# Kernel optimization log

Measured on AMD Instinct MI355X. Metric: run time of the kernel, lower is better.

The kernel has to match this reference:

```python
import jax, jax.numpy as jnp
import numpy as np
import math

B, I, C = 64, 512, 32
PRED, PL, ST, NH = 96, 16, 8, 8
WKS = (24, 168, 336)
PN = (I + ST - PL) // ST + 1  # 64 patches (padding_patch='end')

def _gelu(x):
    return jax.nn.gelu(x, approximate=False)  # torch nn.GELU default (erf)

def _ln(x, g, b, eps=1e-5):
    m = x.mean(-1, keepdims=True)
    v = ((x - m) ** 2).mean(-1, keepdims=True)
    return (x - m) / jnp.sqrt(v + eps) * g + b

def setup_inputs() -> dict:
    keys = jax.random.split(jax.random.key(0), 64)
    ki = iter(keys)
    def nrm(sh, sc=0.02):
        return (jax.random.normal(next(ki), sh) * sc).astype(jnp.float32)
    inp = {}
    inp['s'] = jax.random.normal(next(ki), (B, I, C), jnp.float32)
    inp['t'] = jax.random.normal(next(ki), (B, I, C), jnp.float32)
    inp['cycle_index'] = jax.random.randint(next(ki), (B,), 0, 336)
    # router: Linear(C, C//2) -> GELU -> Linear(C//2, num_scales)
    inp['rw1'] = nrm((C // 2, C)); inp['rb1'] = jnp.zeros(C // 2)
    inp['rw2'] = nrm((3, C // 2)); inp['rb2'] = jnp.zeros(3)
    # per-scale amplitude / phase tables (Wk, C)
    inp['A0'] = nrm((WKS[0], C), 1.0); inp['A1'] = nrm((WKS[1], C), 1.0); inp['A2'] = nrm((WKS[2], C), 1.0)
    inp['P0'] = (jax.random.uniform(next(ki), (WKS[0], C)) * 2 * math.pi).astype(jnp.float32)
    inp['P1'] = (jax.random.uniform(next(ki), (WKS[1], C)) * 2 * math.pi).astype(jnp.float32)
    inp['P2'] = (jax.random.uniform(next(ki), (WKS[2], C)) * 2 * math.pi).astype(jnp.float32)
    # PB_RPA (phase-biased relative patch attention), n_embd=PL, n_head=NH
    inp['Wqkv'] = nrm((3 * PL, PL)); inp['bqkv'] = jnp.zeros(3 * PL)
    inp['Wo'] = nrm((PL, PL)); inp['bo'] = jnp.zeros(PL)
    inp['alpha'] = jnp.ones(())
    # bn2 over channel dim = patch_num
    inp['bn_g'] = jnp.ones(PN); inp['bn_b'] = jnp.zeros(PN)
    inp['W3'] = nrm((2 * PRED, PN * PL)); inp['b3'] = jnp.zeros(2 * PRED)
    inp['W4'] = nrm((PRED, 2 * PRED)); inp['b4'] = jnp.zeros(PRED)
    inp['W5'] = nrm((4 * PRED, I)); inp['b5'] = jnp.zeros(4 * PRED)
    inp['W6'] = nrm((PRED, 2 * PRED)); inp['b6'] = jnp.zeros(PRED)
    inp['W7'] = nrm((PRED, PRED // 2)); inp['b7'] = jnp.zeros(PRED)
    inp['W8'] = nrm((PRED, 2 * PRED)); inp['b8'] = jnp.zeros(PRED)
    inp['ln1_g'] = jnp.ones(2 * PRED); inp['ln1_b'] = jnp.zeros(2 * PRED)
    inp['ln2_g'] = jnp.ones(PRED // 2); inp['ln2_b'] = jnp.zeros(PRED // 2)
    # TrendEnhancer: Conv1d(C, C, 3, pad=1) gated residual
    inp['te_w'] = nrm((C, C, 3)); inp['te_b'] = jnp.zeros(C)
    return inp

def _forward(s, t, cycle_index, rw1, rb1, rw2, rb2, A0, A1, A2, P0, P1, P2,
             Wqkv, bqkv, Wo, bo, alpha, bn_g, bn_b, W3, b3, W4, b4, W5, b5,
             W6, b6, W7, b7, W8, b8, ln1_g, ln1_b, ln2_g, ln2_b, te_w, te_b):
    s = s.transpose(0, 2, 1)  # (B,C,I)
    t = t.transpose(0, 2, 1)
    # router -> per-scale softmax weights (B, num_scales)
    h = _gelu(s.mean(-1) @ rw1.T + rb1)
    p = jax.nn.softmax(h @ rw2.T + rb2, axis=-1)
    ar = jnp.arange(I)
    cs, ps = [], []
    for Atab, Ptab, Wk in ((A0, P0, WKS[0]), (A1, P1, WKS[1]), (A2, P2, WKS[2])):
        idx = (cycle_index[:, None] + ar) % Wk            # (B,I) data-dependent gather
        A = jax.nn.softplus(Atab[idx]).transpose(0, 2, 1)  # (B,C,I)
        phi = Ptab[idx].transpose(0, 2, 1)
        Qr = A * jnp.cos(phi)                              # Qi=A*sin(phi) is unused in hermitian_attn
        S = jnp.einsum('bcl,bck->blk', Qr, s) / math.sqrt(C)
        Aw = jax.nn.softmax(S, axis=-1)
        cs.append(jnp.einsum('blk,bck->bcl', Aw, s))
        ps.append(phi)
    c_stack = jnp.stack(cs, 1)    # (B,3,C,I)
    phi_stack = jnp.stack(ps, 1)
    beta = p[:, :, None, None]
    s = s + (beta * c_stack).sum(1)
    fused_phi = (beta * phi_stack).sum(1)  # (B,C,I)
    N = B * C
    s = s.reshape(N, I)
    t = t.reshape(N, I)
    phi = jnp.repeat(fused_phi.mean(1), C, axis=0)  # (N,I)
    # padding_patch='end' -> replicate-pad last `stride` steps
    s = jnp.concatenate([s, jnp.repeat(s[:, -1:], ST, 1)], 1)
    phi = jnp.concatenate([phi, jnp.repeat(phi[:, -1:], ST, 1)], 1)
    widx = jnp.arange(PN)[:, None] * ST + jnp.arange(PL)
    sp = s[:, widx]                # (N, PN, PL) unfold
    phis = phi[:, widx].mean(-1)   # (N, PN)
    # PB_RPA: MHA over patches with phase-difference bias
    qkv = sp @ Wqkv.T + bqkv
    q, k, v = jnp.split(qkv, 3, axis=-1)
    hd = PL // NH
    def heads(x):
        return x.reshape(N, PN, NH, hd).transpose(0, 2, 1, 3)
    q, k, v = heads(q), heads(k), heads(v)
    bias = alpha * jnp.cos(phis[:, None, :, None] - phis[:, None, None, :])  # (N,1,PN,PN)
    sc = jnp.einsum('nhtd,nhsd->nhts', q, k) / math.sqrt(hd) + bias
    Aw = jax.nn.softmax(sc, axis=-1)
    o = jnp.einsum('nhts,nhsd->nhtd', Aw, v).transpose(0, 2, 1, 3).reshape(N, PN, PL)
    o = o @ Wo.T + bo
    sx = _gelu(sp + o)
    # bn2: BatchNorm1d over channel=patch_num (training-mode batch stats)
    mu = sx.mean((0, 2), keepdims=True)
    var = ((sx - mu) ** 2).mean((0, 2), keepdims=True)
    sx = (sx - mu) / jnp.sqrt(var + 1e-5) * bn_g[None, :, None] + bn_b[None, :, None]
    sx = sx.reshape(N, PN * PL)
    sx = _gelu(sx @ W3.T + b3) @ W4.T + b4  # (N, PRED)
    # trend branch
    u = t @ W5.T + b5                       # (N, 4*PRED)
    u = u.reshape(N, 2 * PRED, 2).mean(-1)  # AvgPool1d(2)
    u = _ln(u, ln1_g, ln1_b)
    u = u @ W6.T + b6
    u = u.reshape(N, PRED // 2, 2).mean(-1)
    u = _ln(u, ln2_g, ln2_b)
    u = u @ W7.T + b7                       # (N, PRED)
    u = u.reshape(B, C, PRED)
    f = jnp.fft.rfft(u, axis=-1)
    mask = (jnp.arange(f.shape[-1]) < 5).astype(f.dtype)
    u = u + jnp.fft.irfft(f * mask, n=PRED, axis=-1)
    y = jax.lax.conv_general_dilated(u, te_w, (1,), [(1, 1)],
                                     dimension_numbers=('NCH', 'OIH', 'NCH')) + te_b[None, :, None]
    u = (u + _gelu(y)).reshape(N, PRED)     # TrendEnhancer gated-conv residual
    x = jnp.concatenate([sx, u], 1) @ W8.T + b8
    return x.reshape(B, C, PRED).transpose(0, 2, 1)  # (B, pred_len, C)

def reference(s, t, cycle_index, rw1, rb1, rw2, rb2, A0, A1, A2, P0, P1, P2,
              Wqkv, bqkv, Wo, bo, alpha, bn_g, bn_b, W3, b3, W4, b4, W5, b5,
              W6, b6, W7, b7, W8, b8, ln1_g, ln1_b, ln2_g, ln2_b, te_w, te_b):
    return _forward(s, t, cycle_index, rw1, rb1, rw2, rb2, A0, A1, A2, P0, P1, P2,
                    Wqkv, bqkv, Wo, bo, alpha, bn_g, bn_b, W3, b3, W4, b4, W5, b5,
                    W6, b6, W7, b7, W8, b8, ln1_g, ln1_b, ln2_g, ln2_b, te_w, te_b)
```

## Files before the change

kernel.cpp:

```cpp
#include <hip/hip_runtime.h>
#include <math.h>

#define B_    64
#define I_    512
#define C_    32
#define PRED_ 96
#define PL_   16
#define ST_   8
#define NH_   8
#define PN_   64
#define N_    2048

typedef short bf16x8 __attribute__((ext_vector_type(8)));
typedef float f32x4 __attribute__((ext_vector_type(4)));
typedef bf16x8 __attribute__((may_alias)) bf16x8_a;
typedef uint2 __attribute__((may_alias)) uint2_a;
typedef uint4 __attribute__((may_alias)) uint4_a;

__device__ __forceinline__ float geluf(float x) {
    return 0.5f * x * (1.0f + erff(x * 0.70710678118654752f));
}
__device__ __forceinline__ float softplusf(float x) {
    return fmaxf(x, 0.0f) + log1pf(__expf(-fabsf(x)));
}
__device__ __forceinline__ unsigned short f2bf(float x) {
    union { float f; unsigned int u; } v; v.f = x;
    unsigned int r = v.u + 0x7fffu + ((v.u >> 16) & 1u);
    return (unsigned short)(r >> 16);
}

__global__ void k_headphi(const float* __restrict__ s, const float* __restrict__ rw1,
                          const float* __restrict__ rb1, const float* __restrict__ rw2,
                          const float* __restrict__ rb2,
                          const float* __restrict__ P0, const float* __restrict__ P1,
                          const float* __restrict__ P2, const int* __restrict__ cyc,
                          float* __restrict__ wp, float* __restrict__ phis) {
    int b = blockIdx.x, t = threadIdx.x;
    __shared__ float part[8][32];
    __shared__ float smean[32];
    __shared__ float h[16];
    __shared__ float wpl[3];
    __shared__ float pm[I_];
    int c = t & 31, chunk = t >> 5;
    float acc = 0.f;
    for (int l = chunk * 64; l < chunk * 64 + 64; ++l)
        acc += s[((size_t)b * I_ + l) * C_ + c];
    part[chunk][c] = acc;
    __syncthreads();
    if (t < 32) {
        float v = 0.f;
#pragma unroll
        for (int i = 0; i < 8; ++i) v += part[i][t];
        smean[t] = v * (1.0f / I_);
    }
    __syncthreads();
    if (t < 16) {
        float a = rb1[t];
#pragma unroll
        for (int c2 = 0; c2 < 32; ++c2) a += smean[c2] * rw1[t * 32 + c2];
        h[t] = geluf(a);
    }
    __syncthreads();
    if (t == 0) {
        float lg[3], mx = -1e30f;
        for (int k = 0; k < 3; ++k) {
            float a = rb2[k];
            for (int j = 0; j < 16; ++j) a += h[j] * rw2[k * 16 + j];
            lg[k] = a; mx = fmaxf(mx, a);
        }
        float d = 0.f;
        for (int k = 0; k < 3; ++k) { lg[k] = __expf(lg[k] - mx); d += lg[k]; }
        float inv = 1.f / d;
        for (int k = 0; k < 3; ++k) { wpl[k] = lg[k] * inv; wp[b * 3 + k] = lg[k] * inv; }
    }
    __syncthreads();
    float p0 = wpl[0], p1 = wpl[1], p2 = wpl[2];
    int cy = cyc[b];
    for (int l = t; l < I_; l += 256) {
        float acc2 = 0.f;
        {
            int idx = (cy + l) % 24;
            const float4* r = (const float4*)(P0 + idx * 32);
            float s4 = 0.f;
#pragma unroll
            for (int i = 0; i < 8; ++i) { float4 v = r[i]; s4 += v.x + v.y + v.z + v.w; }
            acc2 += p0 * s4;
        }
        {
            int idx = (cy + l) % 168;
            const float4* r = (const float4*)(P1 + idx * 32);
            float s4 = 0.f;
#pragma unroll
            for (int i = 0; i < 8; ++i) { float4 v = r[i]; s4 += v.x + v.y + v.z + v.w; }
            acc2 += p1 * s4;
        }
        {
            int idx = (cy + l) % 336;
            const float4* r = (const float4*)(P2 + idx * 32);
            float s4 = 0.f;
#pragma unroll
            for (int i = 0; i < 8; ++i) { float4 v = r[i]; s4 += v.x + v.y + v.z + v.w; }
            acc2 += p2 * s4;
        }
        pm[l] = acc2 * (1.0f / 32.0f);
    }
    __syncthreads();
    if (t < PN_) {
        float sum = 0.f;
#pragma unroll
        for (int j = 0; j < 16; ++j) {
            int l = t * ST_ + j; if (l > 511) l = 511;
            sum += pm[l];
        }
        phis[b * PN_ + t] = sum * (1.0f / 16.0f);
    }
}

__global__ void __launch_bounds__(512) k_attn_mfma(
        const float* __restrict__ s, const int* __restrict__ cyc,
        const float* __restrict__ A0, const float* __restrict__ A1, const float* __restrict__ A2,
        const float* __restrict__ P0, const float* __restrict__ P1, const float* __restrict__ P2,
        const float* __restrict__ wp, float* __restrict__ pcs) {
    int k3 = blockIdx.x, b = blockIdx.y;
    int t = threadIdx.x;
    int wid = t >> 6, lane = t & 63;
    int l15 = lane & 15, lg = lane >> 4;

    __shared__ unsigned short s_lds[512][40];
    __shared__ unsigned short sT[32][520];
    __shared__ unsigned short Pt[8][64][40];

    {
        int row = t;
        const float4* src = (const float4*)(s + ((size_t)b * I_ + row) * C_);
        unsigned short bv[32];
#pragma unroll
        for (int i = 0; i < 8; ++i) {
            float4 v = src[i];
            bv[4 * i + 0] = f2bf(v.x); bv[4 * i + 1] = f2bf(v.y);
            bv[4 * i + 2] = f2bf(v.z); bv[4 * i + 3] = f2bf(v.w);
        }
#pragma unroll
        for (int i = 0; i < 4; ++i) {
            uint4 pk;
            pk.x = (unsigned)bv[8 * i + 0] | ((unsigned)bv[8 * i + 1] << 16);
            pk.y = (unsigned)bv[8 * i + 2] | ((unsigned)bv[8 * i + 3] << 16);
            pk.z = (unsigned)bv[8 * i + 4] | ((unsigned)bv[8 * i + 5] << 16);
            pk.w = (unsigned)bv[8 * i + 6] | ((unsigned)bv[8 * i + 7] << 16);
            *((uint4_a*)&s_lds[row][8 * i]) = pk;
        }
#pragma unroll
        for (int cc = 0; cc < 32; ++cc) sT[cc][row] = bv[cc];
    }

    const float* Atab; const float* Ptab; int Wk;
    if (k3 == 0)      { Atab = A0; Ptab = P0; Wk = 24;  }
    else if (k3 == 1) { Atab = A1; Ptab = P1; Wk = 168; }
    else              { Atab = A2; Ptab = P2; Wk = 336; }
    float wpv = wp[b * 3 + k3];
    int cy = cyc[b];
    bf16x8 qrf[4];
#pragma unroll
    for (int qt = 0; qt < 4; ++qt) {
        int q = wid * 64 + qt * 16 + l15;
        int idx = (cy + q) % Wk;
        const float4* Ar = (const float4*)(Atab + idx * 32 + lg * 8);
        const float4* Pr = (const float4*)(Ptab + idx * 32 + lg * 8);
        float4 a0 = Ar[0], a1 = Ar[1], p0 = Pr[0], p1 = Pr[1];
        float qv[8];
        qv[0] = softplusf(a0.x) * __cosf(p0.x);
        qv[1] = softplusf(a0.y) * __cosf(p0.y);
        qv[2] = softplusf(a0.z) * __cosf(p0.z);
        qv[3] = softplusf(a0.w) * __cosf(p0.w);
        qv[4] = softplusf(a1.x) * __cosf(p1.x);
        qv[5] = softplusf(a1.y) * __cosf(p1.y);
        qv[6] = softplusf(a1.z) * __cosf(p1.z);
        qv[7] = softplusf(a1.w) * __cosf(p1.w);
        bf16x8 f;
#pragma unroll
        for (int j = 0; j < 8; ++j) f[j] = (short)f2bf(qv[j]);
        qrf[qt] = f;
    }
    __syncthreads();

    const float rs = 0.17677669529663687f;
    f32x4 acc[4][2];
#pragma unroll
    for (int qt = 0; qt < 4; ++qt)
#pragma unroll
        for (int ct = 0; ct < 2; ++ct) acc[qt][ct] = (f32x4){0.f, 0.f, 0.f, 0.f};
    float dacc[4] = {0.f, 0.f, 0.f, 0.f};

    for (int kc = 0; kc < 16; ++kc) {
        int key0 = kc * 32;
        bf16x8 a0 = *((const bf16x8_a*)&s_lds[key0 + l15][lg * 8]);
        bf16x8 a1 = *((const bf16x8_a*)&s_lds[key0 + 16 + l15][lg * 8]);
        f32x4 stv[4][2];
#pragma unroll
        for (int qt = 0; qt < 4; ++qt) {
            stv[qt][0] = __builtin_amdgcn_mfma_f32_16x16x32_bf16(a0, qrf[qt], (f32x4){0.f,0.f,0.f,0.f}, 0, 0, 0);
            stv[qt][1] = __builtin_amdgcn_mfma_f32_16x16x32_bf16(a1, qrf[qt], (f32x4){0.f,0.f,0.f,0.f}, 0, 0, 0);
        }
#pragma unroll
        for (int qt = 0; qt < 4; ++qt) {
#pragma unroll
            for (int h = 0; h < 2; ++h) {
                unsigned short pb[4];
                float ds = 0.f;
#pragma unroll
                for (int r = 0; r < 4; ++r) {
                    float e = __expf(stv[qt][h][r] * rs);
                    unsigned short ub = f2bf(e);
                    pb[r] = ub;
                    union { unsigned int u; float f; } bb; bb.u = ((unsigned int)ub) << 16;
                    ds += bb.f;
                }
                dacc[qt] += ds;
                uint2 w2;
                w2.x = (unsigned)pb[0] | ((unsigned)pb[1] << 16);
                w2.y = (unsigned)pb[2] | ((unsigned)pb[3] << 16);
                *((uint2_a*)&Pt[wid][qt * 16 + l15][h * 16 + lg * 4]) = w2;
            }
        }
        bf16x8 b0 = *((const bf16x8_a*)&sT[l15][key0 + lg * 8]);
        bf16x8 b1 = *((const bf16x8_a*)&sT[16 + l15][key0 + lg * 8]);
#pragma unroll
        for (int qt = 0; qt < 4; ++qt) {
            bf16x8 pa = *((const bf16x8_a*)&Pt[wid][qt * 16 + l15][lg * 8]);
            acc[qt][0] = __builtin_amdgcn_mfma_f32_16x16x32_bf16(pa, b0, acc[qt][0], 0, 0, 0);
            acc[qt][1] = __builtin_amdgcn_mfma_f32_16x16x32_bf16(pa, b1, acc[qt][1], 0, 0, 0);
        }
    }

#pragma unroll
    for (int qt = 0; qt < 4; ++qt) {
        float dq = dacc[qt];
        dq += __shfl_xor(dq, 16);
        dq += __shfl_xor(dq, 32);
        float invd[4];
#pragma unroll
        for (int r = 0; r < 4; ++r) {
            float dr = __shfl(dq, 4 * lg + r);
            invd[r] = wpv / dr;
        }
        int qbase = wid * 64 + qt * 16 + 4 * lg;
#pragma unroll
        for (int ct = 0; ct < 2; ++ct) {
            int c = ct * 16 + l15;
            float4 o;
            o.x = acc[qt][ct][0] * invd[0];
            o.y = acc[qt][ct][1] * invd[1];
            o.z = acc[qt][ct][2] * invd[2];
            o.w = acc[qt][ct][3] * invd[3];
            *(float4*)(pcs + (((size_t)k3 * B_ + b) * C_ + c) * I_ + qbase) = o;
        }
    }
}

__global__ void k_combine(const float* __restrict__ s, const float* __restrict__ t,
                          const float* __restrict__ pcs,
                          float* __restrict__ srow, float* __restrict__ trow) {
    int b = blockIdx.x, l0 = blockIdx.y * 32;
    int tt_ = threadIdx.x;
    __shared__ float st[32][33], tl[32][33];
#pragma unroll
    for (int r = 0; r < 4; ++r) {
        int lin = r * 256 + tt_;
        int lq = lin >> 5, c = lin & 31;
        st[lq][c] = s[((size_t)b * I_ + l0 + lq) * C_ + c];
        tl[lq][c] = t[((size_t)b * I_ + l0 + lq) * C_ + c];
    }
    __syncthreads();
    const size_t CH = (size_t)B_ * C_ * I_;
#pragma unroll
    for (int r = 0; r < 4; ++r) {
        int lin = r * 256 + tt_;
        int co = lin >> 5, lo = lin & 31;
        size_t pi = ((size_t)b * C_ + co) * I_ + l0 + lo;
        float sum = pcs[pi] + pcs[CH + pi] + pcs[2 * CH + pi];
        size_t oi = ((size_t)(b * C_ + co)) * I_ + l0 + lo;
        srow[oi] = st[lo][co] + sum;
        trow[oi] = tl[lo][co];
    }
}

__global__ void __launch_bounds__(256) k_patch(
        const float* __restrict__ srow, const float* __restrict__ phis,
        const float* __restrict__ Wqkv, const float* __restrict__ bqkv,
        const float* __restrict__ Wo, const float* __restrict__ bo,
        const float* __restrict__ alpha_p, float* __restrict__ sx) {
    int n = blockIdx.x, t = threadIdx.x;
    int p = t & 63, w = t >> 6;
    int b = n >> 5;
    __shared__ float spl[64][17];
    __shared__ float ql[64][17], kl[64][17], vl[64][17];
    __shared__ float cosl[64], sinl[64];
    __shared__ float wq[48][16];
    __shared__ float wo[16][16];
    __shared__ float o2l[64][17];
    float alpha = alpha_p[0];
    for (int i = t; i < 768; i += 256) wq[i >> 4][i & 15] = Wqkv[i];
    if (t < 256) wo[t >> 4][t & 15] = Wo[t];
    if (t < 64) {
        float sv, cv;
        __sincosf(phis[b * PN_ + t], &sv, &cv);
        cosl[t] = cv; sinl[t] = sv;
    }
    const float* srn = srow + (size_t)n * I_;
#pragma unroll
    for (int jj = 0; jj < 4; ++jj) {
        int j = w * 4 + jj;
        int l = p * ST_ + j; if (l > 511) l = 511;
        spl[p][j] = srn[l];
    }
    __syncthreads();
#pragma unroll
    for (int oo = 0; oo < 12; ++oo) {
        int o = w * 12 + oo;
        float a = bqkv[o];
#pragma unroll
        for (int i2 = 0; i2 < 16; ++i2) a += spl[p][i2] * wq[o][i2];
        if (o < 16) ql[p][o] = a;
        else if (o < 32) kl[p][o - 16] = a;
        else vl[p][o - 32] = a;
    }
    __syncthreads();
    const float rs2 = 0.70710678118654752f;
    float cp = alpha * cosl[p], sp_ = alpha * sinl[p];
#pragma unroll
    for (int hh = 0; hh < 2; ++hh) {
        int h = 2 * w + hh;
        float q0 = ql[p][2 * h] * rs2, q1 = ql[p][2 * h + 1] * rs2;
        float dh = 0.f, o0 = 0.f, o1 = 0.f;
        for (int ss = 0; ss < 64; ++ss) {
            float sc = q0 * kl[ss][2 * h] + q1 * kl[ss][2 * h + 1]
                     + cp * cosl[ss] + sp_ * sinl[ss];
            float e = __expf(sc);
            dh += e; o0 += e * vl[ss][2 * h]; o1 += e * vl[ss][2 * h + 1];
        }
        float inv = 1.f / dh;
        o2l[p][2 * h] = o0 * inv; o2l[p][2 * h + 1] = o1 * inv;
    }
    __syncthreads();
    float* sxr = sx + ((size_t)n * PN_ + p) * PL_;
#pragma unroll
    for (int ii = 0; ii < 4; ++ii) {
        int i2 = w * 4 + ii;
        float a = bo[i2];
#pragma unroll
        for (int j = 0; j < 16; ++j) a += o2l[p][j] * wo[i2][j];
        sxr[i2] = geluf(spl[p][i2] + a);
    }
}

__global__ void k_bn_stats(const float* __restrict__ sx, float* __restrict__ bnpart) {
    int pn = blockIdx.x, chunk = blockIdx.y, t = threadIdx.x;
    __shared__ float r1[256], r2[256];
    int j4 = t & 3, nb = t >> 2;
    float s1 = 0.f, s2 = 0.f;
    for (int i = 0; i < 8; ++i) {
        int n = chunk * 512 + nb + i * 64;
        float4 v = *(const float4*)(sx + ((size_t)n * PN_ + pn) * PL_ + j4 * 4);
        s1 += v.x + v.y + v.z + v.w;
        s2 += v.x * v.x + v.y * v.y + v.z * v.z + v.w * v.w;
    }
    r1[t] = s1; r2[t] = s2;
    __syncthreads();
    for (int st = 128; st > 0; st >>= 1) {
        if (t < st) { r1[t] += r1[t + st]; r2[t] += r2[t + st]; }
        __syncthreads();
    }
    if (t == 0) {
        bnpart[(pn * 4 + chunk) * 2 + 0] = r1[0];
        bnpart[(pn * 4 + chunk) * 2 + 1] = r2[0];
    }
}

__global__ void k_bn_final(const float* __restrict__ bnpart, const float* __restrict__ g,
                           const float* __restrict__ bb, float* __restrict__ bnmul,
                           float* __restrict__ bnadd) {
    int pn = threadIdx.x;
    float s1 = 0.f, s2 = 0.f;
#pragma unroll
    for (int ch = 0; ch < 4; ++ch) {
        s1 += bnpart[(pn * 4 + ch) * 2 + 0];
        s2 += bnpart[(pn * 4 + ch) * 2 + 1];
    }
    const float inv = 1.0f / (N_ * PL_);
    float mu = s1 * inv;
    float var = s2 * inv - mu * mu;
    float m = rsqrtf(var + 1e-5f) * g[pn];
    bnmul[pn] = m;
    bnadd[pn] = bb[pn] - mu * m;
}

template <int ACT, int FUSE_BN>
__global__ void __launch_bounds__(256) k_gemm_mfma(
        const float* __restrict__ A, const float* __restrict__ W,
        const float* __restrict__ bias, const float* __restrict__ bnmul,
        const float* __restrict__ bnadd, float* __restrict__ Cout,
        int M, int Nn, int K) {
    __shared__ unsigned short Ab[64][36];
    __shared__ unsigned short Wb[64][36];
    int bm = blockIdx.x * 64, bn = blockIdx.y * 64;
    int t = threadIdx.x;
    int wid = t >> 6, lane = t & 63, l15 = lane & 15, lg = lane >> 4;
    int srw = t >> 2, sk = (t & 3) * 8;
    f32x4 acc[4];
#pragma unroll
    for (int nt = 0; nt < 4; ++nt) acc[nt] = (f32x4){0.f, 0.f, 0.f, 0.f};

    for (int kt = 0; kt < K; kt += 32) {
        float4 av0 = *(const float4*)(A + (size_t)(bm + srw) * K + kt + sk);
        float4 av1 = *(const float4*)(A + (size_t)(bm + srw) * K + kt + sk + 4);
        float4 wv0 = *(const float4*)(W + (size_t)(bn + srw) * K + kt + sk);
        float4 wv1 = *(const float4*)(W + (size_t)(bn + srw) * K + kt + sk + 4);
        if (FUSE_BN) {
            int pn = (kt + sk) >> 4;
            float m = bnmul[pn], ad = bnadd[pn];
            av0.x = av0.x * m + ad; av0.y = av0.y * m + ad;
            av0.z = av0.z * m + ad; av0.w = av0.w * m + ad;
            av1.x = av1.x * m + ad; av1.y = av1.y * m + ad;
            av1.z = av1.z * m + ad; av1.w = av1.w * m + ad;
        }
        __syncthreads();
        {
            uint4 pk;
            pk.x = (unsigned)f2bf(av0.x) | ((unsigned)f2bf(av0.y) << 16);
            pk.y = (unsigned)f2bf(av0.z) | ((unsigned)f2bf(av0.w) << 16);
            pk.z = (unsigned)f2bf(av1.x) | ((unsigned)f2bf(av1.y) << 16);
            pk.w = (unsigned)f2bf(av1.z) | ((unsigned)f2bf(av1.w) << 16);
            *((uint4_a*)&Ab[srw][sk]) = pk;
            uint4 pw;
            pw.x = (unsigned)f2bf(wv0.x) | ((unsigned)f2bf(wv0.y) << 16);
            pw.y = (unsigned)f2bf(wv0.z) | ((unsigned)f2bf(wv0.w) << 16);
            pw.z = (unsigned)f2bf(wv1.x) | ((unsigned)f2bf(wv1.y) << 16);
            pw.w = (unsigned)f2bf(wv1.z) | ((unsigned)f2bf(wv1.w) << 16);
            *((uint4_a*)&Wb[srw][sk]) = pw;
        }
        __syncthreads();
        bf16x8 af = *((const bf16x8_a*)&Ab[wid * 16 + l15][lg * 8]);
#pragma unroll
        for (int nt = 0; nt < 4; ++nt) {
            bf16x8 wf = *((const bf16x8_a*)&Wb[nt * 16 + l15][lg * 8]);
            acc[nt] = __builtin_amdgcn_mfma_f32_16x16x32_bf16(af, wf, acc[nt], 0, 0, 0);
        }
    }
#pragma unroll
    for (int nt = 0; nt < 4; ++nt) {
#pragma unroll
        for (int r = 0; r < 4; ++r) {
            int m_ = bm + wid * 16 + 4 * lg + r;
            int n_ = bn + nt * 16 + l15;
            float v = acc[nt][r] + bias[n_];
            if (ACT) v = geluf(v);
            Cout[(size_t)m_ * Nn + n_] = v;
        }
    }
}

__global__ void k_rowmlp4(const float* __restrict__ g3, const float* __restrict__ W4,
                          const float* __restrict__ b4, float* __restrict__ sxf) {
    int n = blockIdx.x, t = threadIdx.x;
    __shared__ float row[192];
    for (int j = t; j < 192; j += 128) row[j] = g3[(size_t)n * 192 + j];
    __syncthreads();
    if (t < 96) {
        float a = b4[t];
        const float* wr = W4 + t * 192;
#pragma unroll 4
        for (int j = 0; j < 192; ++j) a += row[j] * wr[j];
        sxf[(size_t)n * 96 + t] = a;
    }
}

__global__ void k_u(const float* __restrict__ u1, const float* __restrict__ ln1g,
                    const float* __restrict__ ln1b, const float* __restrict__ W6,
                    const float* __restrict__ b6, const float* __restrict__ ln2g,
                    const float* __restrict__ ln2b, const float* __restrict__ W7,
                    const float* __restrict__ b7, float* __restrict__ u2out) {
    int n = blockIdx.x, t = threadIdx.x;
    __shared__ float a[192];
    __shared__ float red1[256], red2[256];
    __shared__ float c2[48];
    __shared__ float stat[2];
    __shared__ float u3l[96];
    __shared__ float cosb[5][96], sinb[5][96];
    __shared__ float coef[9];
    if (t < 96) {
#pragma unroll
        for (int k = 0; k < 5; ++k) {
            float sv, cv2;
            __sincosf(6.283185307179586f * (float)(k * t) / 96.0f, &sv, &cv2);
            cosb[k][t] = cv2; sinb[k][t] = sv;
        }
    }
    const float* ur = u1 + (size_t)n * 384;
    float av = 0.5f * (ur[2 * t] + ur[2 * t + 1]);
    red1[t] = av; red2[t] = av * av;
    if (t < 64) { red1[192 + t] = 0.f; red2[192 + t] = 0.f; }
    __syncthreads();
    for (int st = 128; st > 0; st >>= 1) {
        if (t < st) { red1[t] += red1[t + st]; red2[t] += red2[t + st]; }
        __syncthreads();
    }
    if (t == 0) {
        float mu = red1[0] * (1.0f / 192.0f);
        float var = red2[0] * (1.0f / 192.0f) - mu * mu;
        stat[0] = mu; stat[1] = rsqrtf(var + 1e-5f);
    }
    __syncthreads();
    a[t] = (av - stat[0]) * stat[1] * ln1g[t] + ln1b[t];
    __syncthreads();
    float bv = 0.f;
    if (t < 96) {
        bv = b6[t];
        const float* wr = W6 + t * 192;
#pragma unroll 4
        for (int j = 0; j < 192; ++j) bv += a[j] * wr[j];
    }
    __syncthreads();
    if (t < 96) red1[t] = bv;
    __syncthreads();
    float cv = 0.f;
    if (t < 48) cv = 0.5f * (red1[2 * t] + red1[2 * t + 1]);
    __syncthreads();
    if (t < 48) { red1[t] = cv; red2[t] = cv * cv; }
    else if (t < 64) { red1[t] = 0.f; red2[t] = 0.f; }
    __syncthreads();
    for (int st = 32; st > 0; st >>= 1) {
        if (t < st) { red1[t] += red1[t + st]; red2[t] += red2[t + st]; }
        __syncthreads();
    }
    if (t == 0) {
        float mu = red1[0] * (1.0f / 48.0f);
        float var = red2[0] * (1.0f / 48.0f) - mu * mu;
        stat[0] = mu; stat[1] = rsqrtf(var + 1e-5f);
    }
    __syncthreads();
    if (t < 48) c2[t] = (cv - stat[0]) * stat[1] * ln2g[t] + ln2b[t];
    __syncthreads();
    if (t < 96) {
        float acc = b7[t];
        const float* wr = W7 + t * 48;
#pragma unroll
        for (int j = 0; j < 48; ++j) acc += c2[j] * wr[j];
        u3l[t] = acc;
    }
    __syncthreads();
    if (t < 9) {
        int k = (t < 5) ? t : t - 4;
        const float* bas = (t < 5) ? cosb[k] : sinb[k];
        float acc = 0.f;
#pragma unroll 4
        for (int m = 0; m < 96; ++m) acc += u3l[m] * bas[m];
        coef[t] = acc;
    }
    __syncthreads();
    if (t < 96) {
        float rec = coef[0];
#pragma unroll
        for (int k = 1; k <= 4; ++k)
            rec += 2.0f * (coef[k] * cosb[k][t] + coef[4 + k] * sinb[k][t]);
        u2out[(size_t)n * 96 + t] = u3l[t] + rec * (1.0f / 96.0f);
    }
}

__global__ void k_conv(const float* __restrict__ u2, const float* __restrict__ tw,
                       const float* __restrict__ tb, float* __restrict__ u4) {
    int b = blockIdx.x, xq = blockIdx.y, t = threadIdx.x;
    int x0 = xq * 24;
    __shared__ float ub[32][26];
    __shared__ float twl[3072];
    for (int i = t; i < 832; i += 256) {
        int ic = i / 26, xx = i % 26;
        int gx = x0 + xx - 1;
        ub[ic][xx] = (gx >= 0 && gx < 96) ? u2[((size_t)b * 32 + ic) * 96 + gx] : 0.f;
    }
    for (int i = t; i < 3072; i += 256) twl[i] = tw[i];
    __syncthreads();
    for (int i = t; i < 768; i += 256) {
        int oc = i / 24, xx = i % 24;
        float acc = tb[oc];
#pragma unroll 8
        for (int ic = 0; ic < 32; ++ic) {
            const float* wv = twl + (oc * 32 + ic) * 3;
            acc += ub[ic][xx] * wv[0] + ub[ic][xx + 1] * wv[1] + ub[ic][xx + 2] * wv[2];
        }
        u4[((size_t)b * 32 + oc) * 96 + x0 + xx] = ub[oc][xx + 1] + geluf(acc);
    }
}

__global__ void k_out(const float* __restrict__ sxf, const float* __restrict__ u4,
                      const float* __restrict__ W8, const float* __restrict__ b8,
                      float* __restrict__ out) {
    int b = blockIdx.x, oq = blockIdx.y, t = threadIdx.x;
    __shared__ float ld[32][193];
    for (int i = t; i < 32 * 96; i += 256) {
        int c = i / 96, j = i % 96;
        ld[c][j]      = sxf[((size_t)(b * 32 + c)) * 96 + j];
        ld[c][96 + j] = u4[((size_t)(b * 32 + c)) * 96 + j];
    }
    __syncthreads();
    for (int i = t; i < 24 * 32; i += 256) {
        int o = oq * 24 + (i >> 5), c = i & 31;
        float acc = b8[o];
        const float* wr = W8 + o * 192;
#pragma unroll 4
        for (int j = 0; j < 192; ++j) acc += ld[c][j] * wr[j];
        out[((size_t)b * 96 + o) * 32 + c] = acc;
    }
}

extern "C" void kernel_launch(void* const* d_in, const int* in_sizes, int n_in,
                              void* d_out, int out_size, void* d_ws, size_t ws_size,
                              hipStream_t stream) {
    const float* s    = (const float*)d_in[0];
    const float* t    = (const float*)d_in[1];
    const int*   cyc  = (const int*)d_in[2];
    const float* rw1  = (const float*)d_in[3];
    const float* rb1  = (const float*)d_in[4];
    const float* rw2  = (const float*)d_in[5];
    const float* rb2  = (const float*)d_in[6];
    const float* A0   = (const float*)d_in[7];
    const float* A1   = (const float*)d_in[8];
    const float* A2   = (const float*)d_in[9];
    const float* P0   = (const float*)d_in[10];
    const float* P1   = (const float*)d_in[11];
    const float* P2   = (const float*)d_in[12];
    const float* Wqkv = (const float*)d_in[13];
    const float* bqkv = (const float*)d_in[14];
    const float* Wo   = (const float*)d_in[15];
    const float* bo   = (const float*)d_in[16];
    const float* alpha= (const float*)d_in[17];
    const float* bn_g = (const float*)d_in[18];
    const float* bn_b = (const float*)d_in[19];
    const float* W3   = (const float*)d_in[20];
    const float* b3   = (const float*)d_in[21];
    const float* W4   = (const float*)d_in[22];
    const float* b4   = (const float*)d_in[23];
    const float* W5   = (const float*)d_in[24];
    const float* b5   = (const float*)d_in[25];
    const float* W6   = (const float*)d_in[26];
    const float* b6   = (const float*)d_in[27];
    const float* W7   = (const float*)d_in[28];
    const float* b7   = (const float*)d_in[29];
    const float* W8   = (const float*)d_in[30];
    const float* b8   = (const float*)d_in[31];
    const float* ln1g = (const float*)d_in[32];
    const float* ln1b = (const float*)d_in[33];
    const float* ln2g = (const float*)d_in[34];
    const float* ln2b = (const float*)d_in[35];
    const float* tew  = (const float*)d_in[36];
    const float* teb  = (const float*)d_in[37];

    float* ws     = (float*)d_ws;
    float* wp     = ws;
    float* phis   = ws + 192;
    float* bnpart = ws + 4288;
    float* bnmul  = ws + 4800;
    float* bnadd  = ws + 4864;
    float* srow   = ws + 4928;
    float* trow   = srow + 1048576;
    float* R      = trow + 1048576;
    float* pcs = R;
    float* sx  = R;
    float* g3  = R + 2097152;
    float* sxf = R + 2490368;
    float* u1  = R + 2686976;
    float* u2f = R + 3473408;
    float* u4f = R + 3670016;
    float* out = (float*)d_out;

    k_headphi<<<64, 256, 0, stream>>>(s, rw1, rb1, rw2, rb2, P0, P1, P2, cyc, wp, phis);
    k_attn_mfma<<<dim3(3, 64), 512, 0, stream>>>(s, cyc, A0, A1, A2, P0, P1, P2, wp, pcs);
    k_combine<<<dim3(64, 16), 256, 0, stream>>>(s, t, pcs, srow, trow);
    k_patch<<<2048, 256, 0, stream>>>(srow, phis, Wqkv, bqkv, Wo, bo, alpha, sx);
    k_bn_stats<<<dim3(64, 4), 256, 0, stream>>>(sx, bnpart);
    k_bn_final<<<1, 64, 0, stream>>>(bnpart, bn_g, bn_b, bnmul, bnadd);
    k_gemm_mfma<1, 1><<<dim3(32, 3), 256, 0, stream>>>(sx, W3, b3, bnmul, bnadd, g3, 2048, 192, 1024);
    k_rowmlp4<<<2048, 128, 0, stream>>>(g3, W4, b4, sxf);
    k_gemm_mfma<0, 0><<<dim3(32, 6), 256, 0, stream>>>(trow, W5, b5, bnmul, bnadd, u1, 2048, 384, 512);
    k_u<<<2048, 192, 0, stream>>>(u1, ln1g, ln1b, W6, b6, ln2g, ln2b, W7, b7, u2f);
    k_conv<<<dim3(64, 4), 256, 0, stream>>>(u2f, tew, teb, u4f);
    k_out<<<dim3(64, 4), 256, 0, stream>>>(sxf, u4f, W8, b8, out);
}
```

Baseline: 351.6 us.

## Use MFMA for patch attention, fuse BN finalize, read t transposed in GEMM

The patch-attention kernel now computes the QKV projection and the attention scores with bf16 MFMA instructions instead of scalar FP32 loops. The phase bias is folded into the score MFMA as extra K columns. The BN finalize kernel is removed and its per-channel scale and shift are computed inside the GEMM prologue. The t transpose copy is dropped, and the W5 GEMM reads t directly with strided loads. This cuts launches and memory traffic but adds bf16 rounding in attention and uncoalesced strided loads in the second GEMM.

```diff
diff --git a/kernel.cpp b/kernel.cpp
--- a/kernel.cpp
+++ b/kernel.cpp
@@ -257,18 +257,16 @@
     }
 }
 
-__global__ void k_combine(const float* __restrict__ s, const float* __restrict__ t,
-                          const float* __restrict__ pcs,
-                          float* __restrict__ srow, float* __restrict__ trow) {
+__global__ void k_combine(const float* __restrict__ s, const float* __restrict__ pcs,
+                          float* __restrict__ srow) {
     int b = blockIdx.x, l0 = blockIdx.y * 32;
     int tt_ = threadIdx.x;
-    __shared__ float st[32][33], tl[32][33];
+    __shared__ float st[32][33];
 #pragma unroll
     for (int r = 0; r < 4; ++r) {
         int lin = r * 256 + tt_;
         int lq = lin >> 5, c = lin & 31;
         st[lq][c] = s[((size_t)b * I_ + l0 + lq) * C_ + c];
-        tl[lq][c] = t[((size_t)b * I_ + l0 + lq) * C_ + c];
     }
     __syncthreads();
     const size_t CH = (size_t)B_ * C_ * I_;
@@ -278,9 +276,7 @@
         int co = lin >> 5, lo = lin & 31;
         size_t pi = ((size_t)b * C_ + co) * I_ + l0 + lo;
         float sum = pcs[pi] + pcs[CH + pi] + pcs[2 * CH + pi];
-        size_t oi = ((size_t)(b * C_ + co)) * I_ + l0 + lo;
-        srow[oi] = st[lo][co] + sum;
-        trow[oi] = tl[lo][co];
+        srow[pi] = st[lo][co] + sum;
     }
 }
 
@@ -291,57 +287,125 @@
         const float* __restrict__ alpha_p, float* __restrict__ sx) {
     int n = blockIdx.x, t = threadIdx.x;
     int p = t & 63, w = t >> 6;
+    int lane = t & 63, l15 = lane & 15, lg = lane >> 4;
     int b = n >> 5;
     __shared__ float spl[64][17];
-    __shared__ float ql[64][17], kl[64][17], vl[64][17];
-    __shared__ float cosl[64], sinl[64];
-    __shared__ float wq[48][16];
+    __shared__ unsigned short spb[64][16];
+    __shared__ unsigned short wqb[48][16];
+    __shared__ unsigned short qkv2[36][72];
+    __shared__ float vlf[16][68];
+    __shared__ float o2l[64][18];
     __shared__ float wo[16][16];
-    __shared__ float o2l[64][17];
+    const float rs2 = 0.70710678118654752f;
+
     float alpha = alpha_p[0];
-    for (int i = t; i < 768; i += 256) wq[i >> 4][i & 15] = Wqkv[i];
-    if (t < 256) wo[t >> 4][t & 15] = Wo[t];
+    const float* srn = srow + (size_t)n * I_;
+#pragma unroll
+    for (int jj = 0; jj < 4; ++jj) {
+        int j = w * 4 + jj;
+        int l = p * ST_ + j; if (l > 511) l = 511;
+        float v = srn[l];
+        spl[p][j] = v; spb[p][j] = f2bf(v);
+    }
+    for (int i = t; i < 768; i += 256) wqb[i >> 4][i & 15] = f2bf(Wqkv[i]);
+    wo[t >> 4][t & 15] = Wo[t];
     if (t < 64) {
         float sv, cv;
         __sincosf(phis[b * PN_ + t], &sv, &cv);
-        cosl[t] = cv; sinl[t] = sv;
-    }
-    const float* srn = srow + (size_t)n * I_;
-#pragma unroll
-    for (int jj = 0; jj < 4; ++jj) {
-        int j = w * 4 + jj;
-        int l = p * ST_ + j; if (l > 511) l = 511;
-        spl[p][j] = srn[l];
-    }
-    __syncthreads();
-#pragma unroll
-    for (int oo = 0; oo < 12; ++oo) {
-        int o = w * 12 + oo;
-        float a = bqkv[o];
-#pragma unroll
-        for (int i2 = 0; i2 < 16; ++i2) a += spl[p][i2] * wq[o][i2];
-        if (o < 16) ql[p][o] = a;
-        else if (o < 32) kl[p][o - 16] = a;
-        else vl[p][o - 32] = a;
-    }
-    __syncthreads();
-    const float rs2 = 0.70710678118654752f;
-    float cp = alpha * cosl[p], sp_ = alpha * sinl[p];
+        qkv2[32][t] = f2bf(cv); qkv2[33][t] = f2bf(sv);
+        qkv2[34][t] = f2bf(alpha * cv); qkv2[35][t] = f2bf(alpha * sv);
+    }
+    __syncthreads();
+
+    {
+        bf16x8 af = {};
+        if (lg < 2) af = *((const bf16x8_a*)&spb[w * 16 + l15][lg * 8]);
+        f32x4 pacc[3];
+#pragma unroll
+        for (int nt = 0; nt < 3; ++nt) {
+            bf16x8 wf = {};
+            if (lg < 2) wf = *((const bf16x8_a*)&wqb[nt * 16 + l15][lg * 8]);
+            pacc[nt] = __builtin_amdgcn_mfma_f32_16x16x32_bf16(af, wf, (f32x4){0.f,0.f,0.f,0.f}, 0, 0, 0);
+        }
+        __syncthreads();
+#pragma unroll
+        for (int nt = 0; nt < 3; ++nt) {
+            int o = nt * 16 + l15;
+            float bias = bqkv[o];
+            float v0 = pacc[nt][0] + bias, v1 = pacc[nt][1] + bias;
+            float v2 = pacc[nt][2] + bias, v3 = pacc[nt][3] + bias;
+            int pb_ = w * 16 + 4 * lg;
+            if (o < 16) {
+                v0 *= rs2; v1 *= rs2; v2 *= rs2; v3 *= rs2;
+                uint2 w2;
+                w2.x = (unsigned)f2bf(v0) | ((unsigned)f2bf(v1) << 16);
+                w2.y = (unsigned)f2bf(v2) | ((unsigned)f2bf(v3) << 16);
+                *((uint2_a*)&qkv2[o][pb_]) = w2;
+            } else if (o < 32) {
+                uint2 w2;
+                w2.x = (unsigned)f2bf(v0) | ((unsigned)f2bf(v1) << 16);
+                w2.y = (unsigned)f2bf(v2) | ((unsigned)f2bf(v3) << 16);
+                *((uint2_a*)&qkv2[o][pb_]) = w2;
+            } else {
+                *(float4*)&vlf[o - 32][pb_] = make_float4(v0, v1, v2, v3);
+            }
+        }
+    }
+    __syncthreads();
+
 #pragma unroll
     for (int hh = 0; hh < 2; ++hh) {
         int h = 2 * w + hh;
-        float q0 = ql[p][2 * h] * rs2, q1 = ql[p][2 * h + 1] * rs2;
-        float dh = 0.f, o0 = 0.f, o1 = 0.f;
-        for (int ss = 0; ss < 64; ++ss) {
-            float sc = q0 * kl[ss][2 * h] + q1 * kl[ss][2 * h + 1]
-                     + cp * cosl[ss] + sp_ * sinl[ss];
-            float e = __expf(sc);
-            dh += e; o0 += e * vl[ss][2 * h]; o1 += e * vl[ss][2 * h + 1];
-        }
-        float inv = 1.f / dh;
-        o2l[p][2 * h] = o0 * inv; o2l[p][2 * h + 1] = o1 * inv;
-    }
-    __syncthreads();
+        bf16x8 qf[4];
+#pragma unroll
+        for (int pt = 0; pt < 4; ++pt) {
+            bf16x8 f = {};
+            if (lg == 0) {
+                int col = pt * 16 + l15;
+                f[0] = (short)qkv2[2 * h][col];
+                f[1] = (short)qkv2[2 * h + 1][col];
+                f[2] = (short)qkv2[34][col];
+                f[3] = (short)qkv2[35][col];
+            }
+            qf[pt] = f;
+        }
+        float o0a[4] = {0.f,0.f,0.f,0.f}, o1a[4] = {0.f,0.f,0.f,0.f}, da[4] = {0.f,0.f,0.f,0.f};
+#pragma unroll
+        for (int st = 0; st < 4; ++st) {
+            bf16x8 kf = {};
+            if (lg == 0) {
+                int col = st * 16 + l15;
+                kf[0] = (short)qkv2[16 + 2 * h][col];
+                kf[1] = (short)qkv2[17 + 2 * h][col];
+                kf[2] = (short)qkv2[32][col];
+                kf[3] = (short)qkv2[33][col];
+            }
+            float4 v0 = *(const float4*)&vlf[2 * h][st * 16 + 4 * lg];
+            float4 v1 = *(const float4*)&vlf[2 * h + 1][st * 16 + 4 * lg];
+#pragma unroll
+            for (int pt = 0; pt < 4; ++pt) {
+                f32x4 sv = __builtin_amdgcn_mfma_f32_16x16x32_bf16(kf, qf[pt], (f32x4){0.f,0.f,0.f,0.f}, 0, 0, 0);
+                float e0 = __expf(sv[0]), e1 = __expf(sv[1]);
+                float e2 = __expf(sv[2]), e3 = __expf(sv[3]);
+                da[pt] += e0 + e1 + e2 + e3;
+                o0a[pt] += e0 * v0.x + e1 * v0.y + e2 * v0.z + e3 * v0.w;
+                o1a[pt] += e0 * v1.x + e1 * v1.y + e2 * v1.z + e3 * v1.w;
+            }
+        }
+#pragma unroll
+        for (int pt = 0; pt < 4; ++pt) {
+            float o0 = o0a[pt], o1 = o1a[pt], dd = da[pt];
+            o0 += __shfl_xor(o0, 16); o0 += __shfl_xor(o0, 32);
+            o1 += __shfl_xor(o1, 16); o1 += __shfl_xor(o1, 32);
+            dd += __shfl_xor(dd, 16); dd += __shfl_xor(dd, 32);
+            if (lg == 0) {
+                float inv = 1.f / dd;
+                *(float2*)&o2l[pt * 16 + l15][2 * h] = make_float2(o0 * inv, o1 * inv);
+            }
+        }
+    }
+    __syncthreads();
+
     float* sxr = sx + ((size_t)n * PN_ + p) * PL_;
 #pragma unroll
     for (int ii = 0; ii < 4; ++ii) {
@@ -376,48 +440,56 @@
     }
 }
 
-__global__ void k_bn_final(const float* __restrict__ bnpart, const float* __restrict__ g,
-                           const float* __restrict__ bb, float* __restrict__ bnmul,
-                           float* __restrict__ bnadd) {
-    int pn = threadIdx.x;
-    float s1 = 0.f, s2 = 0.f;
-#pragma unroll
-    for (int ch = 0; ch < 4; ++ch) {
-        s1 += bnpart[(pn * 4 + ch) * 2 + 0];
-        s2 += bnpart[(pn * 4 + ch) * 2 + 1];
-    }
-    const float inv = 1.0f / (N_ * PL_);
-    float mu = s1 * inv;
-    float var = s2 * inv - mu * mu;
-    float m = rsqrtf(var + 1e-5f) * g[pn];
-    bnmul[pn] = m;
-    bnadd[pn] = bb[pn] - mu * m;
-}
-
-template <int ACT, int FUSE_BN>
+template <int ACT, int FUSE_BN, int TRANS>
 __global__ void __launch_bounds__(256) k_gemm_mfma(
         const float* __restrict__ A, const float* __restrict__ W,
-        const float* __restrict__ bias, const float* __restrict__ bnmul,
-        const float* __restrict__ bnadd, float* __restrict__ Cout,
-        int M, int Nn, int K) {
+        const float* __restrict__ bias, const float* __restrict__ bnpart,
+        const float* __restrict__ bng, const float* __restrict__ bnb,
+        float* __restrict__ Cout, int M, int Nn, int K) {
     __shared__ unsigned short Ab[64][36];
     __shared__ unsigned short Wb[64][36];
+    __shared__ float bnm[64], bna[64];
     int bm = blockIdx.x * 64, bn = blockIdx.y * 64;
     int t = threadIdx.x;
     int wid = t >> 6, lane = t & 63, l15 = lane & 15, lg = lane >> 4;
     int srw = t >> 2, sk = (t & 3) * 8;
+    if (FUSE_BN && t < 64) {
+        float s1 = 0.f, s2 = 0.f;
+#pragma unroll
+        for (int ch = 0; ch < 4; ++ch) {
+            s1 += bnpart[(t * 4 + ch) * 2 + 0];
+            s2 += bnpart[(t * 4 + ch) * 2 + 1];
+        }
+        const float inv = 1.0f / (N_ * PL_);
+        float mu = s1 * inv;
+        float var = s2 * inv - mu * mu;
+        float m = rsqrtf(var + 1e-5f) * bng[t];
+        bnm[t] = m; bna[t] = bnb[t] - mu * m;
+    }
+    if (FUSE_BN) __syncthreads();
     f32x4 acc[4];
 #pragma unroll
     for (int nt = 0; nt < 4; ++nt) acc[nt] = (f32x4){0.f, 0.f, 0.f, 0.f};
 
     for (int kt = 0; kt < K; kt += 32) {
-        float4 av0 = *(const float4*)(A + (size_t)(bm + srw) * K + kt + sk);
-        float4 av1 = *(const float4*)(A + (size_t)(bm + srw) * K + kt + sk + 4);
+        float4 av0, av1;
+        if (TRANS) {
+            int nrow = bm + srw;
+            const float* tp = A + (size_t)(nrow >> 5) * (I_ * C_) + (nrow & 31);
+            int l0 = kt + sk;
+            av0.x = tp[(size_t)(l0 + 0) * C_]; av0.y = tp[(size_t)(l0 + 1) * C_];
+            av0.z = tp[(size_t)(l0 + 2) * C_]; av0.w = tp[(size_t)(l0 + 3) * C_];
+            av1.x = tp[(size_t)(l0 + 4) * C_]; av1.y = tp[(size_t)(l0 + 5) * C_];
+            av1.z = tp[(size_t)(l0 + 6) * C_]; av1.w = tp[(size_t)(l0 + 7) * C_];
+        } else {
+            av0 = *(const float4*)(A + (size_t)(bm + srw) * K + kt + sk);
+            av1 = *(const float4*)(A + (size_t)(bm + srw) * K + kt + sk + 4);
+        }
         float4 wv0 = *(const float4*)(W + (size_t)(bn + srw) * K + kt + sk);
         float4 wv1 = *(const float4*)(W + (size_t)(bn + srw) * K + kt + sk + 4);
         if (FUSE_BN) {
             int pn = (kt + sk) >> 4;
-            float m = bnmul[pn], ad = bnadd[pn];
+            float m = bnm[pn], ad = bna[pn];
             av0.x = av0.x * m + ad; av0.y = av0.y * m + ad;
             av0.z = av0.z * m + ad; av0.w = av0.w * m + ad;
             av1.x = av1.x * m + ad; av1.y = av1.y * m + ad;
@@ -658,11 +730,8 @@
     float* wp     = ws;
     float* phis   = ws + 192;
     float* bnpart = ws + 4288;
-    float* bnmul  = ws + 4800;
-    float* bnadd  = ws + 4864;
-    float* srow   = ws + 4928;
-    float* trow   = srow + 1048576;
-    float* R      = trow + 1048576;
+    float* srow   = ws + 4800;
+    float* R      = srow + 1048576;
     float* pcs = R;
     float* sx  = R;
     float* g3  = R + 2097152;
@@ -674,13 +743,12 @@
 
     k_headphi<<<64, 256, 0, stream>>>(s, rw1, rb1, rw2, rb2, P0, P1, P2, cyc, wp, phis);
     k_attn_mfma<<<dim3(3, 64), 512, 0, stream>>>(s, cyc, A0, A1, A2, P0, P1, P2, wp, pcs);
-    k_combine<<<dim3(64, 16), 256, 0, stream>>>(s, t, pcs, srow, trow);
+    k_combine<<<dim3(64, 16), 256, 0, stream>>>(s, pcs, srow);
     k_patch<<<2048, 256, 0, stream>>>(srow, phis, Wqkv, bqkv, Wo, bo, alpha, sx);
     k_bn_stats<<<dim3(64, 4), 256, 0, stream>>>(sx, bnpart);
-    k_bn_final<<<1, 64, 0, stream>>>(bnpart, bn_g, bn_b, bnmul, bnadd);
-    k_gemm_mfma<1, 1><<<dim3(32, 3), 256, 0, stream>>>(sx, W3, b3, bnmul, bnadd, g3, 2048, 192, 1024);
+    k_gemm_mfma<1, 1, 0><<<dim3(32, 3), 256, 0, stream>>>(sx, W3, b3, bnpart, bn_g, bn_b, g3, 2048, 192, 1024);
     k_rowmlp4<<<2048, 128, 0, stream>>>(g3, W4, b4, sxf);
-    k_gemm_mfma<0, 0><<<dim3(32, 6), 256, 0, stream>>>(trow, W5, b5, bnmul, bnadd, u1, 2048, 384, 512);
+    k_gemm_mfma<0, 0, 1><<<dim3(32, 6), 256, 0, stream>>>(t, W5, b5, bnpart, bn_g, bn_b, u1, 2048, 384, 512);
     k_u<<<2048, 192, 0, stream>>>(u1, ln1g, ln1b, W6, b6, ln2g, ln2b, W7, b7, u2f);
     k_conv<<<dim3(64, 4), 256, 0, stream>>>(u2f, tew, teb, u4f);
     k_out<<<dim3(64, 4), 256, 0, stream>>>(sxf, u4f, W8, b8, out);
```

After: 341.8 us. -2.8%, faster.
